# Kernel tuning notes

Hardware: AMD Instinct MI355X
Metric: run time of the kernel (lower is better)

Reference implementation:

```python
import jax, jax.numpy as jnp
import numpy as np

N = 40000      # nodes
E = 640000     # edges
G = 2048       # graphs
D = 128        # emb_dim
T = 10         # num_tasks
L = 5          # layers
ATOM_VOCAB = 64
BOND_VOCAB = 8
BN_EPS = 1e-5


def _bn(x, g, b, m, v):
    # inference-mode BatchNorm1d with running stats
    return (x - m) * jax.lax.rsqrt(v + BN_EPS) * g + b


def setup_inputs() -> dict:
    key = jax.random.key(0)
    ks = jax.random.split(key, 24)
    inp = {
        "x_atom": jax.random.randint(ks[0], (N, 9), 0, ATOM_VOCAB),
        "edge_index": jax.random.randint(ks[1], (2, E), 0, N),
        "edge_attr": jax.random.randint(ks[2], (E, 3), 0, BOND_VOCAB),
        "batch": jnp.sort(jax.random.randint(ks[3], (N,), 0, G)),
        # embedding tables
        "atom_emb": jax.random.normal(ks[4], (9, ATOM_VOCAB, D)) * 0.1,
        "bond_emb": jax.random.normal(ks[5], (L, 3, BOND_VOCAB, D)) * 0.1,
        # per-layer GIN params (stacked over L)
        "eps": jnp.zeros((L,)),
        "W1": jax.random.normal(ks[6], (L, D, 2 * D)) * 0.05,
        "b1": jnp.zeros((L, 2 * D)),
        "g1": jnp.ones((L, 2 * D)),
        "bt1": jnp.zeros((L, 2 * D)),
        "m1": jax.random.normal(ks[7], (L, 2 * D)) * 0.1,
        "v1": jax.random.uniform(ks[8], (L, 2 * D), minval=0.5, maxval=1.5),
        "W2": jax.random.normal(ks[9], (L, 2 * D, D)) * 0.05,
        "b2": jnp.zeros((L, D)),
        # outer BatchNorm per layer
        "gO": jnp.ones((L, D)),
        "btO": jnp.zeros((L, D)),
        "mO": jax.random.normal(ks[10], (L, D)) * 0.1,
        "vO": jax.random.uniform(ks[11], (L, D), minval=0.5, maxval=1.5),
        # prediction head
        "Wp": jax.random.normal(ks[12], (D, T)) * 0.05,
        "bp": jnp.zeros((T,)),
    }
    return inp


def reference(x_atom, edge_index, edge_attr, batch, atom_emb, bond_emb, eps,
              W1, b1, g1, bt1, m1, v1, W2, b2, gO, btO, mO, vO, Wp, bp):
    src, dst = edge_index[0], edge_index[1]
    # AtomEncoder: sum of per-feature embeddings -> [N, D]
    x = atom_emb[jnp.arange(9)[None, :], x_atom].sum(axis=1)
    feat3 = jnp.arange(3)[None, :]
    for i in range(L):
        # BondEncoder for this layer -> [E, D]
        e = bond_emb[i][feat3, edge_attr].sum(axis=1)
        # message: relu(x_j + edge_emb); aggregate: scatter-add at dst
        msg = jax.nn.relu(x[src] + e)
        agg = jax.ops.segment_sum(msg, dst, num_segments=N)
        h = (1.0 + eps[i]) * x + agg
        # MLP: Linear -> BN -> ReLU -> Linear
        h = jax.nn.relu(_bn(h @ W1[i] + b1[i], g1[i], bt1[i], m1[i], v1[i]))
        h = h @ W2[i] + b2[i]
        # outer BN; ReLU after all but last layer (dropout = identity in eval)
        x = _bn(h, gO[i], btO[i], mO[i], vO[i])
        if i < L - 1:
            x = jax.nn.relu(x)
    # global mean pool over graphs
    sums = jax.ops.segment_sum(x, batch, num_segments=G)
    cnt = jax.ops.segment_sum(jnp.ones((N,), x.dtype), batch, num_segments=G)
    pooled = sums / jnp.maximum(cnt, 1.0)[:, None]
    return pooled @ Wp + bp
```

## Files before the change

### kernel.cpp

```cpp
#include <hip/hip_runtime.h>
#include <hip/hip_bf16.h>

#define NN 40000
#define NE 640000
#define NG 2048
#define DD 128
#define NT 10
#define NL 5
#define NB 80

typedef __attribute__((ext_vector_type(8))) short short8;
typedef __attribute__((ext_vector_type(8))) float f32x8;
typedef __attribute__((ext_vector_type(4))) float f32x4;
typedef unsigned short ushort_t;
typedef unsigned char uchar_t;

static __device__ __forceinline__ ushort_t f2b(float f) {
    return __bfloat16_as_ushort(__float2bfloat16(f));
}
static __device__ __forceinline__ float b2f(ushort_t u) {
    return __bfloat162float(__ushort_as_bfloat16(u));
}
static __device__ __forceinline__ uchar_t f2p8(float f) {
    return (uchar_t)(__builtin_amdgcn_cvt_pk_fp8_f32(f, 0.f, 0, false) & 0xFF);
}

__global__ void __launch_bounds__(256)
k_setup(const float* __restrict__ W1, const float* __restrict__ W2,
        const float* __restrict__ bemb, const int* __restrict__ xa,
        const float* __restrict__ aemb, const int* __restrict__ ei,
        ushort_t* __restrict__ W1P, ushort_t* __restrict__ W2P,
        ushort_t* __restrict__ ebsum16, ushort_t* __restrict__ x16,
        uchar_t* __restrict__ x8, int* __restrict__ deg) {
    int b = blockIdx.x, t = threadIdx.x;
    if (b < 1280) {
        int tid = b * 256 + t;
        int layer = tid >> 16;
        int r = tid & 65535;
        int half = r >> 15;
        int q = r & 32767;
        int j = q & 7;
        int lane = (q >> 3) & 63;
        if (half == 0) {
            int kk = (q >> 9) & 3;
            int nt = q >> 11;
            int n = nt * 16 + (lane & 15);
            int k = kk * 32 + (lane >> 4) * 8 + j;
            W1P[layer * 32768 + q] = f2b(W1[(layer * DD + k) * 256 + n]);
        } else {
            int kk = (q >> 9) & 7;
            int nt = q >> 12;
            int n = nt * 16 + (lane & 15);
            int k = kk * 32 + (lane >> 4) * 8 + j;
            W2P[layer * 32768 + q] = f2b(W2[(layer * 256 + k) * DD + n]);
        }
        int d = tid & 127;
        int c = (tid >> 7) & 511;
        const float* bl = bemb + (size_t)layer * 3 * 8 * DD;
        ebsum16[tid] = f2b(bl[(c & 7) * DD + d] + bl[(8 + ((c >> 3) & 7)) * DD + d] +
                           bl[(16 + (c >> 6)) * DD + d]);
    } else if (b < 3780) {
        int bb = b - 1280;
        __shared__ int idxS[144];
        if (t < 144) idxS[t] = xa[bb * 144 + t];
        __syncthreads();
        int nl = t >> 4, dcol = t & 15;
        int n = bb * 16 + nl;
        float acc[8];
#pragma unroll
        for (int k = 0; k < 8; ++k) acc[k] = 0.f;
#pragma unroll
        for (int f = 0; f < 9; ++f) {
            const f32x8 v = *(const f32x8*)&aemb[(f * 64 + idxS[nl * 9 + f]) * DD + dcol * 8];
#pragma unroll
            for (int k = 0; k < 8; ++k) acc[k] += v[k];
        }
        short8 o16;
#pragma unroll
        for (int k = 0; k < 8; ++k) o16[k] = (short)f2b(acc[k]);
        *(short8*)&x16[(size_t)n * DD + dcol * 8] = o16;
        unsigned int lo = 0, hi = 0;
        lo = __builtin_amdgcn_cvt_pk_fp8_f32(acc[0], acc[1], lo, false);
        lo = __builtin_amdgcn_cvt_pk_fp8_f32(acc[2], acc[3], lo, true);
        hi = __builtin_amdgcn_cvt_pk_fp8_f32(acc[4], acc[5], hi, false);
        hi = __builtin_amdgcn_cvt_pk_fp8_f32(acc[6], acc[7], hi, true);
        *(uint2*)&x8[(size_t)n * DD + dcol * 8] = make_uint2(lo, hi);
    } else {
        int e = (b - 3780) * 256 + t;
        atomicAdd(&deg[ei[NE + e]], 1);
    }
}


__global__ void k_scan1(const int* __restrict__ deg, int* __restrict__ off,
                        int* __restrict__ blksum) {
    int b = blockIdx.x, t = threadIdx.x;
    int i = b * 256 + t;
    __shared__ int s[256];
    int v = (i < NN) ? deg[i] : 0;
    s[t] = v;
    __syncthreads();
    for (int d = 1; d < 256; d <<= 1) {
        int add = (t >= d) ? s[t - d] : 0;
        __syncthreads();
        s[t] += add;
        __syncthreads();
    }
    if (i <= NN) off[i] = s[t] - v;
    if (t == 255) blksum[b] = s[255];
}

__global__ void k_scan2(int* __restrict__ blk) {
    int t = threadIdx.x;
    __shared__ int s[256];
    int v = blk[t];
    s[t] = v;
    __syncthreads();
    for (int d = 1; d < 256; d <<= 1) {
        int add = (t >= d) ? s[t - d] : 0;
        __syncthreads();
        s[t] += add;
        __syncthreads();
    }
    blk[256 + t] = s[t] - v;
}

__global__ void k_scan3(int* __restrict__ off, const int* __restrict__ blk) {
    int b = blockIdx.x, t = threadIdx.x;
    int i = b * 256 + t;
    if (i <= NN) off[i] += blk[256 + b];
}

__global__ void __launch_bounds__(256)
k_bucket(const int* __restrict__ ei, const int* __restrict__ ea,
         const int* __restrict__ off, int* __restrict__ gbk,
         int2* __restrict__ ebuf) {
    __shared__ int hist[NB];
    __shared__ int sbase[NB];
    int t = threadIdx.x;
    int e0 = blockIdx.x * 1024;
    if (t < NB) hist[t] = 0;
    __syncthreads();
    int rank[4], buck[4], rec[4], dstv[4];
#pragma unroll
    for (int k = 0; k < 4; ++k) {
        int e = e0 + k * 256 + t;
        int src = ei[e];
        int dst = ei[NE + e];
        int a0 = ea[e * 3 + 0], a1 = ea[e * 3 + 1], a2 = ea[e * 3 + 2];
        rec[k] = src | ((a0 | (a1 << 3) | (a2 << 6)) << 16);
        dstv[k] = dst;
        int b = dst >> 9;
        buck[k] = b;
        rank[k] = atomicAdd(&hist[b], 1);
    }
    __syncthreads();
    if (t < NB) sbase[t] = atomicAdd(&gbk[t], hist[t]);
    __syncthreads();
#pragma unroll
    for (int k = 0; k < 4; ++k) {
        int b = buck[k];
        int slot = off[b << 9] + sbase[b] + rank[k];
        ebuf[slot] = make_int2(rec[k], dstv[k]);
    }
}

__global__ void k_scatter2(const int2* __restrict__ ebuf, const int* __restrict__ off,
                           int* __restrict__ cursor, int* __restrict__ epack) {
    int i = blockIdx.x * 256 + threadIdx.x;
    int2 s = ebuf[i];
    int dst = s.y;
    int p = off[dst] + atomicAdd(&cursor[dst], 1);
    epack[p] = s.x;
}

__global__ void __launch_bounds__(256)
k_gather(const ushort_t* __restrict__ xin, const uchar_t* __restrict__ x8in,
         const int* __restrict__ off, const int* __restrict__ epack,
         const ushort_t* __restrict__ ebsum16, const float* __restrict__ eps,
         int layer, ushort_t* __restrict__ h16) {
    int t = threadIdx.x;
    int lane = t & 63;
    int n = blockIdx.x * 4 + (t >> 6);
    const ushort2* x2 = (const ushort2*)xin;
    const ushort_t* x8r = (const ushort_t*)x8in;
    const ushort2* eb2 = (const ushort2*)ebsum16;
    ushort2 xv = x2[n * 64 + lane];
    float es = 1.f + eps[layer];
    float ax = es * b2f(xv.x), ay = es * b2f(xv.y);
    int p = off[n], p1 = off[n + 1];

    int e[8], f[8];
    bool have = (p + 8 <= p1);
    if (have) {
#pragma unroll
        for (int k = 0; k < 8; ++k) e[k] = epack[p + k];
    }
    while (have) {
        int np = p + 8;
        bool nh = (np + 8 <= p1);
        if (nh) {
#pragma unroll
            for (int k = 0; k < 8; ++k) f[k] = epack[np + k];
        }
        ushort2 vv[8];
        ushort_t sp[8];
#pragma unroll
        for (int k = 0; k < 8; ++k) {
            vv[k] = eb2[(e[k] >> 16) * 64 + lane];
            sp[k] = x8r[(e[k] & 0xFFFF) * 64 + lane];
        }
#pragma unroll
        for (int k = 0; k < 8; ++k) {
            float sx = __builtin_amdgcn_cvt_f32_fp8((int)sp[k], 0);
            float sy = __builtin_amdgcn_cvt_f32_fp8((int)sp[k], 1);
            ax += fmaxf(b2f(vv[k].x) + sx, 0.f);
            ay += fmaxf(b2f(vv[k].y) + sy, 0.f);
        }
        p = np;
#pragma unroll
        for (int k = 0; k < 8; ++k) e[k] = f[k];
        have = nh;
    }
    if (p + 4 <= p1) {
        int e4[4];
#pragma unroll
        for (int k = 0; k < 4; ++k) e4[k] = epack[p + k];
        ushort2 vv[4];
        ushort_t sp[4];
#pragma unroll
        for (int k = 0; k < 4; ++k) {
            vv[k] = eb2[(e4[k] >> 16) * 64 + lane];
            sp[k] = x8r[(e4[k] & 0xFFFF) * 64 + lane];
        }
#pragma unroll
        for (int k = 0; k < 4; ++k) {
            float sx = __builtin_amdgcn_cvt_f32_fp8((int)sp[k], 0);
            float sy = __builtin_amdgcn_cvt_f32_fp8((int)sp[k], 1);
            ax += fmaxf(b2f(vv[k].x) + sx, 0.f);
            ay += fmaxf(b2f(vv[k].y) + sy, 0.f);
        }
        p += 4;
    }
    for (; p < p1; ++p) {
        int er = epack[p];
        ushort2 ev = eb2[(er >> 16) * 64 + lane];
        ushort_t sv = x8r[(er & 0xFFFF) * 64 + lane];
        ax += fmaxf(b2f(ev.x) + __builtin_amdgcn_cvt_f32_fp8((int)sv, 0), 0.f);
        ay += fmaxf(b2f(ev.y) + __builtin_amdgcn_cvt_f32_fp8((int)sv, 1), 0.f);
    }
    ushort2 o;
    o.x = f2b(ax);
    o.y = f2b(ay);
    ((ushort2*)h16)[n * 64 + lane] = o;
}

__global__ void __launch_bounds__(256)
k_mlp_mfma(const ushort_t* __restrict__ h16, const ushort_t* __restrict__ W1P,
           const ushort_t* __restrict__ W2P, const float* __restrict__ b1,
           const float* __restrict__ g1, const float* __restrict__ bt1,
           const float* __restrict__ m1, const float* __restrict__ v1,
           const float* __restrict__ b2_, const float* __restrict__ gO,
           const float* __restrict__ btO, const float* __restrict__ mO,
           const float* __restrict__ vO, int relu, ushort_t* __restrict__ xout,
           uchar_t* __restrict__ x8out) {
    __shared__ ushort_t aS[32 * 136];
    __shared__ ushort_t mid[32 * 264];
    int t = threadIdx.x;
    int wave = t >> 6, lane = t & 63;
    int row0 = blockIdx.x * 32;
    int lrow = lane & 15, quad = lane >> 4;

#pragma unroll
    for (int ps = 0; ps < 2; ++ps) {
        int idx = ps * 256 + t;
        int r = idx >> 4, c = (idx & 15) * 8;
        *(short8*)&aS[r * 136 + c] = *(const short8*)&h16[(row0 + r) * DD + c];
    }
    __syncthreads();

    f32x4 acc1[2][4];
#pragma unroll
    for (int rt = 0; rt < 2; ++rt)
#pragma unroll
        for (int i = 0; i < 4; ++i) acc1[rt][i] = (f32x4){0.f, 0.f, 0.f, 0.f};
#pragma unroll
    for (int kk = 0; kk < 4; ++kk) {
        short8 af0 = *(const short8*)&aS[lrow * 136 + kk * 32 + quad * 8];
        short8 af1 = *(const short8*)&aS[(16 + lrow) * 136 + kk * 32 + quad * 8];
#pragma unroll
        for (int i = 0; i < 4; ++i) {
            int nt = wave * 4 + i;
            short8 bf = *(const short8*)&W1P[((nt * 4 + kk) * 64 + lane) * 8];
            acc1[0][i] = __builtin_amdgcn_mfma_f32_16x16x32_bf16(af0, bf, acc1[0][i], 0, 0, 0);
            acc1[1][i] = __builtin_amdgcn_mfma_f32_16x16x32_bf16(af1, bf, acc1[1][i], 0, 0, 0);
        }
    }
    __syncthreads();
#pragma unroll
    for (int i = 0; i < 4; ++i) {
        int col = (wave * 4 + i) * 16 + lrow;
        float s1 = g1[col] * rsqrtf(v1[col] + 1e-5f);
        float sh = bt1[col] - (m1[col] - b1[col]) * s1;
#pragma unroll
        for (int rt = 0; rt < 2; ++rt)
#pragma unroll
            for (int r = 0; r < 4; ++r) {
                int row = rt * 16 + quad * 4 + r;
                float o = acc1[rt][i][r] * s1 + sh;
                mid[row * 264 + col] = f2b(fmaxf(o, 0.f));
            }
    }
    __syncthreads();

    f32x4 acc2[2][2];
#pragma unroll
    for (int rt = 0; rt < 2; ++rt)
#pragma unroll
        for (int i = 0; i < 2; ++i) acc2[rt][i] = (f32x4){0.f, 0.f, 0.f, 0.f};
#pragma unroll
    for (int kk = 0; kk < 8; ++kk) {
        short8 af0 = *(const short8*)&mid[lrow * 264 + kk * 32 + quad * 8];
        short8 af1 = *(const short8*)&mid[(16 + lrow) * 264 + kk * 32 + quad * 8];
#pragma unroll
        for (int i = 0; i < 2; ++i) {
            int nt = wave * 2 + i;
            short8 bf = *(const short8*)&W2P[((nt * 8 + kk) * 64 + lane) * 8];
            acc2[0][i] = __builtin_amdgcn_mfma_f32_16x16x32_bf16(af0, bf, acc2[0][i], 0, 0, 0);
            acc2[1][i] = __builtin_amdgcn_mfma_f32_16x16x32_bf16(af1, bf, acc2[1][i], 0, 0, 0);
        }
    }
    uchar_t* s8 = (uchar_t*)aS;
#pragma unroll
    for (int i = 0; i < 2; ++i) {
        int col = (wave * 2 + i) * 16 + lrow;
        float s = gO[col] * rsqrtf(vO[col] + 1e-5f);
        float sh = btO[col] - (mO[col] - b2_[col]) * s;
#pragma unroll
        for (int rt = 0; rt < 2; ++rt)
#pragma unroll
            for (int r = 0; r < 4; ++r) {
                int row = rt * 16 + quad * 4 + r;
                float o = acc2[rt][i][r] * s + sh;
                if (relu) o = fmaxf(o, 0.f);
                xout[(row0 + row) * DD + col] = f2b(o);
                s8[row * DD + col] = f2p8(o);
            }
    }
    __syncthreads();
    ((int4*)(x8out + (size_t)row0 * DD))[t] = ((const int4*)s8)[t];
}

__global__ void k_poolhead(const ushort_t* __restrict__ x16,
                           const int* __restrict__ batch,
                           const float* __restrict__ Wp, const float* __restrict__ bp,
                           float* __restrict__ out) {
    int g = blockIdx.x, d = threadIdx.x;
    int lo = 0, hi = NN;
    while (lo < hi) { int m = (lo + hi) >> 1; if (batch[m] < g) lo = m + 1; else hi = m; }
    int start = lo;
    hi = NN;
    while (lo < hi) { int m = (lo + hi) >> 1; if (batch[m] < g + 1) lo = m + 1; else hi = m; }
    int end = lo;
    float s = 0.f;
    for (int n = start; n < end; ++n) s += b2f(x16[n * DD + d]);
    float c = fmaxf((float)(end - start), 1.f);
    __shared__ float p[DD];
    p[d] = s / c;
    __syncthreads();
    if (d < NT) {
        float acc = bp[d];
#pragma unroll 8
        for (int k = 0; k < DD; ++k) acc = fmaf(p[k], Wp[k * NT + d], acc);
        out[g * NT + d] = acc;
    }
}

extern "C" void kernel_launch(void* const* d_in, const int* in_sizes, int n_in,
                              void* d_out, int out_size, void* d_ws, size_t ws_size,
                              hipStream_t stream) {
    const int* x_atom = (const int*)d_in[0];
    const int* edge_index = (const int*)d_in[1];
    const int* edge_attr = (const int*)d_in[2];
    const int* batch = (const int*)d_in[3];
    const float* atom_emb = (const float*)d_in[4];
    const float* bond_emb = (const float*)d_in[5];
    const float* eps = (const float*)d_in[6];
    const float* W1 = (const float*)d_in[7];
    const float* b1 = (const float*)d_in[8];
    const float* g1 = (const float*)d_in[9];
    const float* bt1 = (const float*)d_in[10];
    const float* m1 = (const float*)d_in[11];
    const float* v1 = (const float*)d_in[12];
    const float* W2 = (const float*)d_in[13];
    const float* b2 = (const float*)d_in[14];
    const float* gO = (const float*)d_in[15];
    const float* btO = (const float*)d_in[16];
    const float* mO = (const float*)d_in[17];
    const float* vO = (const float*)d_in[18];
    const float* Wp = (const float*)d_in[19];
    const float* bp = (const float*)d_in[20];

    ushort_t* x16a = (ushort_t*)d_ws;
    ushort_t* x16b = x16a + NN * DD;
    ushort_t* h16 = x16b + NN * DD;
    ushort_t* W1P = h16 + NN * DD;
    ushort_t* W2P = W1P + NL * 32768;
    ushort_t* ebsum16 = W2P + NL * 32768;
    uchar_t* x8a = (uchar_t*)(ebsum16 + NL * 65536);
    uchar_t* x8b = x8a + NN * DD;
    int* deg = (int*)(x8b + NN * DD);
    int* off = deg + NN;
    int* blk = off + 40064;
    int* cursor = blk + 512;
    int* gbk = cursor + NN;
    int* epack = gbk + 128;
    int2* ebuf = (int2*)(epack + NE);

    hipMemsetAsync(deg, 0, (NN + 40064 + 512 + NN + 128) * sizeof(int), stream);

    k_setup<<<6280, 256, 0, stream>>>(W1, W2, bond_emb, x_atom, atom_emb,
                                      edge_index, W1P, W2P, ebsum16, x16a, x8a, deg);
    k_scan1<<<157, 256, 0, stream>>>(deg, off, blk);
    k_scan2<<<1, 256, 0, stream>>>(blk);
    k_scan3<<<157, 256, 0, stream>>>(off, blk);
    k_bucket<<<NE / 1024, 256, 0, stream>>>(edge_index, edge_attr, off, gbk, ebuf);
    k_scatter2<<<NE / 256, 256, 0, stream>>>(ebuf, off, cursor, epack);

    for (int i = 0; i < NL; ++i) {
        ushort_t* xin = (i & 1) ? x16b : x16a;
        ushort_t* xout = (i & 1) ? x16a : x16b;
        uchar_t* x8in = (i & 1) ? x8b : x8a;
        uchar_t* x8out = (i & 1) ? x8a : x8b;
        k_gather<<<NN / 4, 256, 0, stream>>>(xin, x8in, off, epack,
                                             ebsum16 + i * 65536, eps, i, h16);
        k_mlp_mfma<<<NN / 32, 256, 0, stream>>>(
            h16, W1P + (size_t)i * 32768, W2P + (size_t)i * 32768, b1 + i * 256,
            g1 + i * 256, bt1 + i * 256, m1 + i * 256, v1 + i * 256, b2 + i * DD,
            gO + i * DD, btO + i * DD, mO + i * DD, vO + i * DD,
            (i < NL - 1) ? 1 : 0, xout, x8out);
    }
    k_poolhead<<<NG, DD, 0, stream>>>(x16b, batch, Wp, bp, (float*)d_out);
}
```

Baseline: 406.0 us.

## Replace global degree scan with per-bucket histogram and block-local CSR build

CSR construction no longer counts a global per-node degree with atomics and then runs a three-kernel prefix scan. It now counts edges per 512-node bucket using shared-memory histograms and scans the 80 bucket totals. A new per-bucket kernel computes the node offsets and scatters the edges into the packed array, using shared-memory counts and cursors. This removes two launches, most global atomics and a large memset, but the CSR scatter now runs on only 80 blocks, which limits parallelism in that stage.

```diff
diff --git a/kernel.cpp b/kernel.cpp
--- a/kernel.cpp
+++ b/kernel.cpp
@@ -31,7 +31,7 @@
         const float* __restrict__ aemb, const int* __restrict__ ei,
         ushort_t* __restrict__ W1P, ushort_t* __restrict__ W2P,
         ushort_t* __restrict__ ebsum16, ushort_t* __restrict__ x16,
-        uchar_t* __restrict__ x8, int* __restrict__ deg) {
+        uchar_t* __restrict__ x8, int* __restrict__ gcnt) {
     int b = blockIdx.x, t = threadIdx.x;
     if (b < 1280) {
         int tid = b * 256 + t;
@@ -86,54 +86,38 @@
         hi = __builtin_amdgcn_cvt_pk_fp8_f32(acc[6], acc[7], hi, true);
         *(uint2*)&x8[(size_t)n * DD + dcol * 8] = make_uint2(lo, hi);
     } else {
-        int e = (b - 3780) * 256 + t;
-        atomicAdd(&deg[ei[NE + e]], 1);
-    }
-}
-
-
-__global__ void k_scan1(const int* __restrict__ deg, int* __restrict__ off,
-                        int* __restrict__ blksum) {
-    int b = blockIdx.x, t = threadIdx.x;
-    int i = b * 256 + t;
-    __shared__ int s[256];
-    int v = (i < NN) ? deg[i] : 0;
+        __shared__ int hist[NB];
+        int e0 = (b - 3780) * 1024;
+        if (t < NB) hist[t] = 0;
+        __syncthreads();
+#pragma unroll
+        for (int k = 0; k < 4; ++k) {
+            int e = e0 + k * 256 + t;
+            atomicAdd(&hist[ei[NE + e] >> 9], 1);
+        }
+        __syncthreads();
+        if (t < NB) atomicAdd(&gcnt[t], hist[t]);
+    }
+}
+
+__global__ void k_bscan(const int* __restrict__ gcnt, int* __restrict__ bbase) {
+    int t = threadIdx.x;
+    __shared__ int s[128];
+    int v = (t < NB) ? gcnt[t] : 0;
     s[t] = v;
     __syncthreads();
-    for (int d = 1; d < 256; d <<= 1) {
+    for (int d = 1; d < 128; d <<= 1) {
         int add = (t >= d) ? s[t - d] : 0;
         __syncthreads();
         s[t] += add;
         __syncthreads();
     }
-    if (i <= NN) off[i] = s[t] - v;
-    if (t == 255) blksum[b] = s[255];
-}
-
-__global__ void k_scan2(int* __restrict__ blk) {
-    int t = threadIdx.x;
-    __shared__ int s[256];
-    int v = blk[t];
-    s[t] = v;
-    __syncthreads();
-    for (int d = 1; d < 256; d <<= 1) {
-        int add = (t >= d) ? s[t - d] : 0;
-        __syncthreads();
-        s[t] += add;
-        __syncthreads();
-    }
-    blk[256 + t] = s[t] - v;
-}
-
-__global__ void k_scan3(int* __restrict__ off, const int* __restrict__ blk) {
-    int b = blockIdx.x, t = threadIdx.x;
-    int i = b * 256 + t;
-    if (i <= NN) off[i] += blk[256 + b];
+    if (t <= NB) bbase[t] = s[t] - v;
 }
 
 __global__ void __launch_bounds__(256)
 k_bucket(const int* __restrict__ ei, const int* __restrict__ ea,
-         const int* __restrict__ off, int* __restrict__ gbk,
+         const int* __restrict__ bbase, int* __restrict__ gbk,
          int2* __restrict__ ebuf) {
     __shared__ int hist[NB];
     __shared__ int sbase[NB];
@@ -160,18 +144,47 @@
 #pragma unroll
     for (int k = 0; k < 4; ++k) {
         int b = buck[k];
-        int slot = off[b << 9] + sbase[b] + rank[k];
+        int slot = bbase[b] + sbase[b] + rank[k];
         ebuf[slot] = make_int2(rec[k], dstv[k]);
     }
 }
 
-__global__ void k_scatter2(const int2* __restrict__ ebuf, const int* __restrict__ off,
-                           int* __restrict__ cursor, int* __restrict__ epack) {
-    int i = blockIdx.x * 256 + threadIdx.x;
-    int2 s = ebuf[i];
-    int dst = s.y;
-    int p = off[dst] + atomicAdd(&cursor[dst], 1);
-    epack[p] = s.x;
+__global__ void __launch_bounds__(256)
+k_csr(const int2* __restrict__ ebuf, const int* __restrict__ bbase,
+      int* __restrict__ off, int* __restrict__ epack) {
+    __shared__ int cnt[512];
+    __shared__ int cur[512];
+    __shared__ int sc[256];
+    int b = blockIdx.x, t = threadIdx.x;
+    int base = bbase[b], end = bbase[b + 1];
+    cnt[t] = 0; cnt[t + 256] = 0;
+    cur[t] = 0; cur[t + 256] = 0;
+    __syncthreads();
+    for (int i = base + t; i < end; i += 256)
+        atomicAdd(&cnt[ebuf[i].y & 511], 1);
+    __syncthreads();
+    int a = cnt[2 * t], c2 = cnt[2 * t + 1];
+    sc[t] = a + c2;
+    __syncthreads();
+    for (int d = 1; d < 256; d <<= 1) {
+        int add = (t >= d) ? sc[t - d] : 0;
+        __syncthreads();
+        sc[t] += add;
+        __syncthreads();
+    }
+    int ex = sc[t] - (a + c2);
+    cnt[2 * t] = ex;
+    cnt[2 * t + 1] = ex + a;
+    int n0 = (b << 9) + 2 * t;
+    if (n0 <= NN) off[n0] = base + ex;
+    if (n0 + 1 <= NN) off[n0 + 1] = base + ex + a;
+    __syncthreads();
+    for (int i = base + t; i < end; i += 256) {
+        int2 s = ebuf[i];
+        int l = s.y & 511;
+        int r = atomicAdd(&cur[l], 1);
+        epack[base + cnt[l] + r] = s.x;
+    }
 }
 
 __global__ void __launch_bounds__(256)
@@ -409,23 +422,20 @@
     ushort_t* ebsum16 = W2P + NL * 32768;
     uchar_t* x8a = (uchar_t*)(ebsum16 + NL * 65536);
     uchar_t* x8b = x8a + NN * DD;
-    int* deg = (int*)(x8b + NN * DD);
-    int* off = deg + NN;
-    int* blk = off + 40064;
-    int* cursor = blk + 512;
-    int* gbk = cursor + NN;
-    int* epack = gbk + 128;
+    int* off = (int*)(x8b + NN * DD);
+    int* gcnt = off + 40064;
+    int* gbk = gcnt + 80;
+    int* bbase = gbk + 80;
+    int* epack = bbase + 128;
     int2* ebuf = (int2*)(epack + NE);
 
-    hipMemsetAsync(deg, 0, (NN + 40064 + 512 + NN + 128) * sizeof(int), stream);
-
-    k_setup<<<6280, 256, 0, stream>>>(W1, W2, bond_emb, x_atom, atom_emb,
-                                      edge_index, W1P, W2P, ebsum16, x16a, x8a, deg);
-    k_scan1<<<157, 256, 0, stream>>>(deg, off, blk);
-    k_scan2<<<1, 256, 0, stream>>>(blk);
-    k_scan3<<<157, 256, 0, stream>>>(off, blk);
-    k_bucket<<<NE / 1024, 256, 0, stream>>>(edge_index, edge_attr, off, gbk, ebuf);
-    k_scatter2<<<NE / 256, 256, 0, stream>>>(ebuf, off, cursor, epack);
+    hipMemsetAsync(gcnt, 0, 160 * sizeof(int), stream);
+
+    k_setup<<<4405, 256, 0, stream>>>(W1, W2, bond_emb, x_atom, atom_emb,
+                                      edge_index, W1P, W2P, ebsum16, x16a, x8a, gcnt);
+    k_bscan<<<1, 128, 0, stream>>>(gcnt, bbase);
+    k_bucket<<<NE / 1024, 256, 0, stream>>>(edge_index, edge_attr, bbase, gbk, ebuf);
+    k_csr<<<NB, 256, 0, stream>>>(ebuf, bbase, off, epack);
 
     for (int i = 0; i < NL; ++i) {
         ushort_t* xin = (i & 1) ? x16b : x16a;
```

New measurement: 383.2 us. -5.6%, faster.
